# Optimization experiments

Hardware: AMD Instinct MI355X
Metric: run time of the kernel (lower is better)

Reference implementation:

```python
import jax, jax.numpy as jnp
import numpy as np

B, S, D_IN, H, BLOCKS, OUT_DIM = 32, 128, 16, 128, 3, 1
TAU = 0.5
BN_EPS = 1e-5


def _conv1d(x, w, b, dil):
    # x: [B, C, S], w: [O, I, K], 'same' padding with dilation (matches torch padding='same')
    y = jax.lax.conv_general_dilated(x, w, (1,), 'SAME', rhs_dilation=(dil,),
                                     dimension_numbers=('NCH', 'OIH', 'NCH'))
    return y + b[None, :, None]


def setup_inputs() -> dict:
    key = jax.random.key(0)
    ks = jax.random.split(key, 24)
    w = lambda k, shape, s=0.05: (jax.random.normal(k, shape, jnp.float32) * s)
    return {
        'data': jax.random.normal(ks[0], (B, S, D_IN), jnp.float32),
        'gumbel_u': jax.random.uniform(ks[1], (B, S * S, 2), jnp.float32),
        'w11': w(ks[2], (H, D_IN, 1)), 'b11': jnp.zeros((H,), jnp.float32),
        'w12': w(ks[3], (H, H, 3)),    'b12': jnp.zeros((H,), jnp.float32),
        'w21': w(ks[4], (H, D_IN, 1)), 'b21': jnp.zeros((H,), jnp.float32),
        'w22': w(ks[5], (H, H, 5)),    'b22': jnp.zeros((H,), jnp.float32),
        'w31': w(ks[6], (H, D_IN, 1)), 'b31': jnp.zeros((H,), jnp.float32),
        'wf': w(ks[7], (3 * H, H)),    'bf': jnp.zeros((H,), jnp.float32),
        'w1': w(ks[8], (2 * H, H)),    'b1': jnp.zeros((H,), jnp.float32),
        'w2': w(ks[9], (H, 2)),        'b2': jnp.zeros((2,), jnp.float32),
        'wl': w(ks[10], (BLOCKS, H, H)), 'bl': jnp.zeros((BLOCKS, H), jnp.float32),
        'wr': w(ks[11], (BLOCKS, H, H)),
        'gamma': jnp.ones((BLOCKS, H), jnp.float32), 'beta': jnp.zeros((BLOCKS, H), jnp.float32),
        'wg': w(ks[12], (BLOCKS, 1), 0.3), 'bg': jnp.zeros((1,), jnp.float32),
        'we': w(ks[13], (H, H // 2)),  'be': jnp.zeros((H // 2,), jnp.float32),
        'wo': w(ks[14], (H // 2, OUT_DIM)), 'bo': jnp.zeros((OUT_DIM,), jnp.float32),
    }


def reference(data, gumbel_u, w11, b11, w12, b12, w21, b21, w22, b22, w31, b31,
              wf, bf, w1, b1, w2, b2, wl, bl, wr, gamma, beta, wg, bg, we, be, wo, bo):
    b_, s_, _ = data.shape
    xd = jnp.transpose(data, (0, 2, 1))                    # [B, D_IN, S]
    # dilated TCN feature extraction
    x1 = _conv1d(_conv1d(xd, w11, b11, 1), w12, b12, 3)
    x2 = _conv1d(_conv1d(xd, w21, b21, 1), w22, b22, 5)
    x3 = _conv1d(xd, w31, b31, 1)
    x = jnp.concatenate([x1, x2, x3], axis=1)              # [B, 3H, S]
    x = jnp.transpose(x, (0, 2, 1))                        # [B, S, 3H]
    x = jax.nn.relu(x @ wf + bf)                           # [B, S, H] node features

    # edge scoring: pair (i,j) gets cat(sender=x[j], receiver=x[i]); fc1 split avoids [B,S,S,2H]
    hs = x @ w1[:H]                                        # sender part  [B, S, H]
    hr = x @ w1[H:]                                        # receiver part [B, S, H]
    h = jax.nn.relu(hs[:, None, :, :] + hr[:, :, None, :] + b1)  # [B, S(i), S(j), H]
    logits = h @ w2 + b2                                   # [B, S, S, 2]

    # hard gumbel-softmax, channel 0 = edge on
    u = jnp.clip(gumbel_u, 1e-6, 1.0 - 1e-6).reshape(b_, s_, s_, 2)
    g = -jnp.log(-jnp.log(u))
    y = (logits + g) / TAU
    adj = (jnp.argmax(y, axis=-1) == 0).astype(x.dtype)    # [B, S, S]
    # zero strict lower triangle (tri_mask) and diagonal (keep_self_loops=False)
    idx = jnp.arange(s_)
    adj = adj * (idx[None, :] > idx[:, None])[None]
    # edge_list in torch is non-differentiable -> no grad through adjacency
    adj = jax.lax.stop_gradient(adj)

    # SAGEConv (mean aggr) + BatchNorm, dense per-sample message passing
    deg = jnp.maximum(adj.sum(axis=1), 1.0)                # in-degree of target j, [B, S]
    xn = x
    outs = []
    for l in range(BLOCKS):
        agg = jnp.einsum('bij,bih->bjh', adj, xn) / deg[..., None]
        out = agg @ wl[l] + bl[l] + xn @ wr[l]             # lin_l(agg) + lin_r(x)
        m = out.mean(axis=(0, 1))
        v = out.var(axis=(0, 1))
        xn = (out - m) * jax.lax.rsqrt(v + BN_EPS) * gamma[l] + beta[l]
        outs.append(xn)

    stk = jnp.stack(outs, axis=-1)                          # [B, S, H, BLOCKS]
    xw = jax.nn.relu(jnp.einsum('bshk,ko->bsh', stk, wg) + bg[0])
    last = xw[:, -1]                                        # aggregate='last' -> [B, H]
    h2 = jax.nn.relu(last @ we + be)
    return h2 @ wo + bo                                     # [B, OUT_DIM]
```

## Files before the change

### kernel.cpp

```cpp
#include <hip/hip_runtime.h>
#include <math.h>

#define BB 32
#define SS 128
#define DIN 16
#define HH 128
#define NBSH (BB*SS*HH)

typedef __attribute__((ext_vector_type(8))) short short8;
typedef __attribute__((ext_vector_type(4))) float vf4;

__device__ __forceinline__ float4 f4fma(float s, float4 w, float4 c){
    return make_float4(fmaf(s,w.x,c.x), fmaf(s,w.y,c.y), fmaf(s,w.z,c.z), fmaf(s,w.w,c.w));
}
__device__ __forceinline__ unsigned short f2bf(float x){
    union { float f; unsigned int u; } v; v.f = x;
    unsigned int r = v.u + 0x7FFF + ((v.u >> 16) & 1);
    return (unsigned short)(r >> 16);
}
__device__ __forceinline__ float bf2f(unsigned short b){
    union { unsigned int u; float f; } v; v.u = ((unsigned int)b) << 16;
    return v.f;
}

__global__ __launch_bounds__(256) void k_prep(
    const float* __restrict__ w12, const float* __restrict__ w22,
    const float* __restrict__ w31,
    const float* __restrict__ w11, const float* __restrict__ b11,
    const float* __restrict__ w21, const float* __restrict__ b21,
    const float* __restrict__ wl, const float* __restrict__ wr,
    float* __restrict__ W3, float* __restrict__ W5, float* __restrict__ W31T,
    float* __restrict__ Beff1, float* __restrict__ Beff2, float* __restrict__ accf,
    unsigned short* __restrict__ wHi, unsigned short* __restrict__ wLo)
{
    __shared__ float W12L[8*384];
    __shared__ float W22L[8*640];
    __shared__ float w11L[2048], w21L[2048], b11L[128], b21L[128];
    int blk = blockIdx.x; int tid = threadIdx.x;

    if (blk < 16){
        int h0 = blk*8;
        for (int i = tid; i < 768; i += 256){
            int hl = i/96, o4 = i%96;
            *reinterpret_cast<float4*>(W12L + hl*384 + o4*4) =
                reinterpret_cast<const float4*>(w12)[(h0+hl)*96 + o4];
        }
        for (int i = tid; i < 1280; i += 256){
            int hl = i/160, o4 = i%160;
            *reinterpret_cast<float4*>(W22L + hl*640 + o4*4) =
                reinterpret_cast<const float4*>(w22)[(h0+hl)*160 + o4];
        }
        for (int i = tid; i < 512; i += 256)
            *reinterpret_cast<float4*>(w11L + i*4) = reinterpret_cast<const float4*>(w11)[i];
        for (int i = tid; i < 512; i += 256)
            *reinterpret_cast<float4*>(w21L + i*4) = reinterpret_cast<const float4*>(w21)[i];
        if (tid < 128){ b11L[tid] = b11[tid]; b21L[tid] = b21[tid]; }
        if (blk == 0){ for (int i = tid; i < 768; i += 256) accf[i] = 0.f; }
        __syncthreads();

        for (int T = tid; T < 1216; T += 256){
            if (T < 384){
                int hl = T/48, kd = T%48, k = kd>>4, d = kd&15;
                float a = 0.f;
                #pragma unroll 4
                for (int c = 0; c < HH; ++c) a = fmaf(W12L[hl*384 + c*3 + k], w11L[c*16 + d], a);
                W3[(k*16+d)*128 + h0+hl] = a;
            } else if (T < 1024){
                int tt = T-384, hl = tt/80, kd = tt%80, k = kd>>4, d = kd&15;
                float a = 0.f;
                #pragma unroll 4
                for (int c = 0; c < HH; ++c) a = fmaf(W22L[hl*640 + c*5 + k], w21L[c*16 + d], a);
                W5[(k*16+d)*128 + h0+hl] = a;
            } else if (T < 1048){
                int tt = T-1024, hl = tt/3, k = tt%3;
                float a = 0.f;
                #pragma unroll 4
                for (int c = 0; c < HH; ++c) a = fmaf(W12L[hl*384 + c*3 + k], b11L[c], a);
                Beff1[k*128 + h0+hl] = a;
            } else if (T < 1088){
                int tt = T-1048, hl = tt/5, k = tt%5;
                float a = 0.f;
                #pragma unroll 4
                for (int c = 0; c < HH; ++c) a = fmaf(W22L[hl*640 + c*5 + k], b21L[c], a);
                Beff2[k*128 + h0+hl] = a;
            } else {
                int tt = T-1088, hl = tt>>4, d = tt&15;
                W31T[d*128 + h0+hl] = w31[(h0+hl)*16 + d];
            }
        }
    } else {
        int q = blk - 16;
        int h = tid & 127; int half = tid >> 7;
        for (int rl = half; rl < 32; rl += 2){
            int r = q*32 + rl;
            int m = r >> 7;
            int c = r & 127;
            const float* src = (m < 3) ? (wl + (size_t)m*16384) : (wr + (size_t)(m-3)*16384);
            float v = src[c*128 + h];
            unsigned short hi = f2bf(v);
            unsigned short lo = f2bf(v - bf2f(hi));
            wHi[(size_t)m*16384 + h*128 + c] = hi;
            wLo[(size_t)m*16384 + h*128 + c] = lo;
        }
    }
}

__global__ __launch_bounds__(256) void k_fuse_all(
    const float* __restrict__ data,
    const float* __restrict__ W3, const float* __restrict__ W5,
    const float* __restrict__ W31T,
    const float* __restrict__ Beff1, const float* __restrict__ Beff2,
    const float* __restrict__ b12, const float* __restrict__ b22,
    const float* __restrict__ b31,
    const float* __restrict__ wf, const float* __restrict__ bf,
    const float* __restrict__ w1, const float* __restrict__ b1,
    float* __restrict__ hs, float* __restrict__ hrT, float* __restrict__ XT)
{
    __shared__ __align__(16) float sb[11648];
    float* At   = sb;
    float* Wt   = sb + 6912;
    float* dinT = sb + 11008;
    int blk = blockIdx.x; int row0 = blk*16;
    int b = row0 >> 7; int s0 = row0 & 127;
    int tid = threadIdx.x; int h = tid & 127; int g = tid >> 7;

    for (int idx = tid; idx < 576; idx += 256){
        int r = idx >> 4, d = idx & 15;
        int sp = s0 - 10 + r;
        dinT[d*40 + r] = (sp >= 0 && sp < SS) ? data[(b*SS+sp)*DIN + d] : 0.f;
    }
    __syncthreads();

    float a1[8], a2[8], a3[8];
    #pragma unroll
    for (int m = 0; m < 8; ++m){ a1[m]=0.f; a2[m]=0.f; a3[m]=0.f; }
    for (int d = 0; d < DIN; ++d){
        float w3v[3], w5v[5];
        #pragma unroll
        for (int k = 0; k < 3; ++k) w3v[k] = W3[(k*DIN+d)*HH + h];
        #pragma unroll
        for (int k = 0; k < 5; ++k) w5v[k] = W5[(k*DIN+d)*HH + h];
        float w31v = W31T[d*HH + h];
        const float* dp = dinT + d*40;
        #pragma unroll
        for (int sub = 0; sub < 2; ++sub){
            int rb = g*8 + sub*4;
            const float4* qp = reinterpret_cast<const float4*>(dp + rb);
            float4 q0=qp[0],q1=qp[1],q2=qp[2],q3=qp[3],q4=qp[4],q5=qp[5];
            float qf[24] = {q0.x,q0.y,q0.z,q0.w, q1.x,q1.y,q1.z,q1.w,
                            q2.x,q2.y,q2.z,q2.w, q3.x,q3.y,q3.z,q3.w,
                            q4.x,q4.y,q4.z,q4.w, q5.x,q5.y,q5.z,q5.w};
            #pragma unroll
            for (int tp = 0; tp < 4; ++tp){
                int m = sub*4 + tp;
                #pragma unroll
                for (int k = 0; k < 3; ++k) a1[m] = fmaf(qf[tp+3*k+7], w3v[k], a1[m]);
                #pragma unroll
                for (int k = 0; k < 5; ++k) a2[m] = fmaf(qf[tp+5*k], w5v[k], a2[m]);
                a3[m] = fmaf(qf[tp+10], w31v, a3[m]);
            }
        }
    }
    {
        float be1[3] = {Beff1[h], Beff1[HH+h], Beff1[2*HH+h]};
        float be2[5] = {Beff2[h], Beff2[HH+h], Beff2[2*HH+h], Beff2[3*HH+h], Beff2[4*HH+h]};
        float bv12 = b12[h], bv22 = b22[h], bv31 = b31[h];
        #pragma unroll
        for (int m = 0; m < 8; ++m){
            int rl = g*8 + m;
            int s = s0 + rl;
            float v1 = a1[m] + bv12;
            #pragma unroll
            for (int k = 0; k < 3; ++k)
                if ((unsigned)(s + 3*k - 3) < SS) v1 += be1[k];
            float v2 = a2[m] + bv22;
            #pragma unroll
            for (int k = 0; k < 5; ++k)
                if ((unsigned)(s + 5*k - 10) < SS) v2 += be2[k];
            At[h*18 + rl]        = v1;
            At[(HH+h)*18 + rl]   = v2;
            At[(2*HH+h)*18 + rl] = a3[m] + bv31;
        }
    }
    __syncthreads();

    int r0 = (tid>>5)*2, c0 = (tid&31)*4;
    float4 facc[2] = {{0,0,0,0},{0,0,0,0}};
    for (int ch = 0; ch < 12; ++ch){
        int kk0 = ch*32;
        #pragma unroll
        for (int u = 0; u < 4; ++u){
            int k = (tid>>5) + 8*u;
            *reinterpret_cast<float4*>(Wt + k*128 + c0) =
                *reinterpret_cast<const float4*>(wf + (size_t)(kk0+k)*128 + c0);
        }
        __syncthreads();
        #pragma unroll 4
        for (int k = 0; k < 32; ++k){
            float2 a = *reinterpret_cast<const float2*>(At + (kk0+k)*18 + r0);
            float4 w = *reinterpret_cast<const float4*>(Wt + k*128 + c0);
            facc[0] = f4fma(a.x, w, facc[0]);
            facc[1] = f4fma(a.y, w, facc[1]);
        }
        __syncthreads();
    }
    float* xT = sb;
    float* Wb = sb + 2304;
    float* Wa = sb + 6912;
    {
        float4 bf4 = *reinterpret_cast<const float4*>(bf + c0);
        #pragma unroll
        for (int u = 0; u < 2; ++u){
            float4 v = make_float4(fmaxf(facc[u].x+bf4.x,0.f), fmaxf(facc[u].y+bf4.y,0.f),
                                   fmaxf(facc[u].z+bf4.z,0.f), fmaxf(facc[u].w+bf4.w,0.f));
            xT[(c0+0)*18 + r0+u] = v.x;
            xT[(c0+1)*18 + r0+u] = v.y;
            xT[(c0+2)*18 + r0+u] = v.z;
            xT[(c0+3)*18 + r0+u] = v.w;
        }
    }
    __syncthreads();

    float4 as[2] = {{0,0,0,0},{0,0,0,0}};
    float4 ar[2] = {{0,0,0,0},{0,0,0,0}};
    for (int ch = 0; ch < 4; ++ch){
        int ck0 = ch*32;
        #pragma unroll
        for (int u = 0; u < 4; ++u){
            int k = (tid>>5) + 8*u;
            *reinterpret_cast<float4*>(Wa + k*128 + c0) =
                *reinterpret_cast<const float4*>(w1 + (size_t)(ck0+k)*128 + c0);
            *reinterpret_cast<float4*>(Wb + k*128 + c0) =
                *reinterpret_cast<const float4*>(w1 + (size_t)(128+ck0+k)*128 + c0);
        }
        __syncthreads();
        #pragma unroll 4
        for (int k = 0; k < 32; ++k){
            float2 a = *reinterpret_cast<const float2*>(xT + (ck0+k)*18 + r0);
            float4 wa = *reinterpret_cast<const float4*>(Wa + k*128 + c0);
            float4 wb = *reinterpret_cast<const float4*>(Wb + k*128 + c0);
            as[0]=f4fma(a.x,wa,as[0]); ar[0]=f4fma(a.x,wb,ar[0]);
            as[1]=f4fma(a.y,wa,as[1]); ar[1]=f4fma(a.y,wb,ar[1]);
        }
        __syncthreads();
    }
    float4 b14 = *reinterpret_cast<const float4*>(b1 + c0);
    int rin = s0 + r0;
    #pragma unroll
    for (int u = 0; u < 2; ++u){
        *reinterpret_cast<float4*>(hs + (size_t)(row0+r0+u)*128 + c0) =
            make_float4(as[u].x, as[u].y, as[u].z, as[u].w);
        hrT[((size_t)b*HH + c0+0)*SS + rin+u] = ar[u].x + b14.x;
        hrT[((size_t)b*HH + c0+1)*SS + rin+u] = ar[u].y + b14.y;
        hrT[((size_t)b*HH + c0+2)*SS + rin+u] = ar[u].z + b14.z;
        hrT[((size_t)b*HH + c0+3)*SS + rin+u] = ar[u].w + b14.w;
    }
    for (int idx = tid; idx < 2048; idx += 256){
        int c = idx >> 4, s = idx & 15;
        XT[((size_t)(b*HH + c))*SS + s0 + s] = xT[c*18 + s];
    }
}

__global__ __launch_bounds__(256) void k_adj(
    const float* __restrict__ hs, const float* __restrict__ hrT,
    const float* __restrict__ w2, const float* __restrict__ b2,
    const float* __restrict__ gu, unsigned short* __restrict__ adjT,
    float* __restrict__ deginv)
{
    int blk = blockIdx.x; int b = blk >> 4; int j0 = (blk & 15) * 8;
    int tid = threadIdx.x; int i = tid & 127; int g = tid >> 7;
    __shared__ float hsL[8][128];
    __shared__ float w20L[128], w21L[128];
    __shared__ int degS[8];
    for (int idx = tid; idx < 1024; idx += 256){
        int jj = idx >> 7, h = idx & 127;
        hsL[jj][h] = hs[(size_t)(b*SS + j0 + jj)*HH + h];
    }
    if (tid < 128){ w20L[tid] = w2[tid*2]; w21L[tid] = w2[tid*2+1]; }
    if (tid < 8) degS[tid] = 0;
    __syncthreads();
    float d0[4] = {0,0,0,0}, d1[4] = {0,0,0,0};
    const float* hrb = hrT + (size_t)b*HH*SS + i;
    #pragma unroll 4
    for (int h = 0; h < 128; ++h){
        float hrv = hrb[(size_t)h*SS];
        float wa = w20L[h], wb = w21L[h];
        float r0 = fmaxf(hsL[g*4+0][h] + hrv, 0.f);
        float r1 = fmaxf(hsL[g*4+1][h] + hrv, 0.f);
        float r2 = fmaxf(hsL[g*4+2][h] + hrv, 0.f);
        float r3 = fmaxf(hsL[g*4+3][h] + hrv, 0.f);
        d0[0]=fmaf(r0,wa,d0[0]); d1[0]=fmaf(r0,wb,d1[0]);
        d0[1]=fmaf(r1,wa,d0[1]); d1[1]=fmaf(r1,wb,d1[1]);
        d0[2]=fmaf(r2,wa,d0[2]); d1[2]=fmaf(r2,wb,d1[2]);
        d0[3]=fmaf(r3,wa,d0[3]); d1[3]=fmaf(r3,wb,d1[3]);
    }
    float b20 = b2[0], b21 = b2[1];
    #pragma unroll
    for (int jj = 0; jj < 4; ++jj){
        int j = j0 + g*4 + jj;
        size_t e = (size_t)(b*SS + i)*SS + j;
        float2 uv = *reinterpret_cast<const float2*>(gu + e*2);
        float u0 = fminf(fmaxf(uv.x, 1e-6f), 0.999999f);
        float u1 = fminf(fmaxf(uv.y, 1e-6f), 0.999999f);
        float g0 = -logf(-logf(u0));
        float g1 = -logf(-logf(u1));
        float y0 = d0[jj] + b20 + g0;
        float y1 = d1[jj] + b21 + g1;
        bool av = (j > i) && (y0 >= y1);
        adjT[(size_t)(b*SS + j)*SS + i] = av ? (unsigned short)0x3F80 : (unsigned short)0;
        unsigned long long msk = __ballot(av);
        if ((tid & 63) == 0) atomicAdd(&degS[g*4+jj], (int)__popcll(msk));
    }
    __syncthreads();
    if (tid < 8) deginv[b*SS + j0 + tid] = 1.f / fmaxf((float)degS[tid], 1.f);
}

#define AGGH 0
#define AGGL 4352
#define ADJA 8704
#define XH   13056
#define XL   22272
#define LINA 8704
#define XNJH 29184
#define XNJL 33536
__global__ __launch_bounds__(512) void k_gnn(
    const unsigned short* __restrict__ adjT, const float* __restrict__ xnT,
    const float* __restrict__ deginv,
    const float* __restrict__ gammaP, const float* __restrict__ betaP,
    const float* __restrict__ accP, int aff,
    const unsigned short* __restrict__ wlH, const unsigned short* __restrict__ wlL,
    const unsigned short* __restrict__ wrH, const unsigned short* __restrict__ wrL,
    const float* __restrict__ bl,
    float* __restrict__ outT, float* __restrict__ accL)
{
    __shared__ __align__(16) unsigned short pool[37888];
    __shared__ float2 scsh[128];
    __shared__ float dinvL[32];
    __shared__ float2 redS[128];
    __shared__ float blL[128];
    int blk = blockIdx.x; int b = blk >> 2; int j0 = (blk & 3) * 32;
    int tid = threadIdx.x; int lane = tid & 63; int w = tid >> 6;
    int frow = lane & 15, fk = (lane >> 4) * 8;

    if (tid < 128){
        if (aff){
            float2 s = reinterpret_cast<const float2*>(accP)[tid];
            float m = s.x * (1.f/4096.f);
            float var = fmaxf(s.y * (1.f/4096.f) - m*m, 0.f);
            float sc = gammaP[tid] / sqrtf(var + 1e-5f);
            scsh[tid] = make_float2(sc, betaP[tid] - m*sc);
        } else scsh[tid] = make_float2(1.f, 0.f);
        redS[tid] = make_float2(0.f, 0.f);
        blL[tid] = bl[tid];
    }
    if (tid < 32) dinvL[tid] = deginv[b*SS + j0 + tid];
    __syncthreads();

    {
        int jl = tid >> 4, c8 = tid & 15;
        *reinterpret_cast<uint4*>(pool + ADJA + jl*136 + c8*8) =
            *reinterpret_cast<const uint4*>(adjT + ((size_t)(b*SS + j0 + jl))*SS + c8*8);
    }

    int mt = w & 1, ntb = (w >> 1) * 2;
    vf4 acc[2]; acc[0]=0.f; acc[1]=0.f;
    for (int cs = 0; cs < 2; ++cs){
        for (int task = tid; task < 2048; task += 512){
            int hh = task >> 4, q = task & 15;
            float4 v = *reinterpret_cast<const float4*>(
                xnT + ((size_t)(b*HH + hh))*SS + cs*64 + q*4);
            float2 ss = scsh[hh];
            float e0 = fmaf(v.x, ss.x, ss.y), e1 = fmaf(v.y, ss.x, ss.y);
            float e2 = fmaf(v.z, ss.x, ss.y), e3 = fmaf(v.w, ss.x, ss.y);
            unsigned short h0 = f2bf(e0), h1 = f2bf(e1), h2 = f2bf(e2), h3 = f2bf(e3);
            unsigned int hA = (unsigned int)h0 | ((unsigned int)h1 << 16);
            unsigned int hB = (unsigned int)h2 | ((unsigned int)h3 << 16);
            unsigned short l0 = f2bf(e0 - bf2f(h0)), l1 = f2bf(e1 - bf2f(h1));
            unsigned short l2 = f2bf(e2 - bf2f(h2)), l3 = f2bf(e3 - bf2f(h3));
            unsigned int lA = (unsigned int)l0 | ((unsigned int)l1 << 16);
            unsigned int lB = (unsigned int)l2 | ((unsigned int)l3 << 16);
            *reinterpret_cast<uint2*>(pool + XH + hh*72 + q*4) = make_uint2(hA, hB);
            *reinterpret_cast<uint2*>(pool + XL + hh*72 + q*4) = make_uint2(lA, lB);
        }
        __syncthreads();
        #pragma unroll
        for (int ks = 0; ks < 2; ++ks){
            short8 af = *reinterpret_cast<const short8*>(
                pool + ADJA + (mt*16 + frow)*136 + cs*64 + ks*32 + fk);
            #pragma unroll
            for (int ntl = 0; ntl < 2; ++ntl){
                int nt = ntb + ntl;
                short8 bh = *reinterpret_cast<const short8*>(
                    pool + XH + (nt*16 + frow)*72 + ks*32 + fk);
                short8 bo = *reinterpret_cast<const short8*>(
                    pool + XL + (nt*16 + frow)*72 + ks*32 + fk);
                acc[ntl] = __builtin_amdgcn_mfma_f32_16x16x32_bf16(af, bh, acc[ntl], 0, 0, 0);
                acc[ntl] = __builtin_amdgcn_mfma_f32_16x16x32_bf16(af, bo, acc[ntl], 0, 0, 0);
            }
        }
        __syncthreads();
    }
    #pragma unroll
    for (int ntl = 0; ntl < 2; ++ntl){
        int hh = (ntb + ntl)*16 + frow;
        #pragma unroll
        for (int r = 0; r < 4; ++r){
            int jl = mt*16 + (lane>>4)*4 + r;
            float v = acc[ntl][r] * dinvL[jl];
            unsigned short hi = f2bf(v);
            pool[AGGH + jl*136 + hh] = hi;
            pool[AGGL + jl*136 + hh] = f2bf(v - bf2f(hi));
        }
    }
    if (tid < 256){
        int jg = tid >> 5, cg = tid & 31;
        float mv[4][4];
        #pragma unroll
        for (int e = 0; e < 4; ++e){
            float4 v = *reinterpret_cast<const float4*>(
                xnT + ((size_t)(b*HH + cg*4 + e))*SS + j0 + jg*4);
            float2 ss = scsh[cg*4 + e];
            mv[e][0]=fmaf(v.x,ss.x,ss.y); mv[e][1]=fmaf(v.y,ss.x,ss.y);
            mv[e][2]=fmaf(v.z,ss.x,ss.y); mv[e][3]=fmaf(v.w,ss.x,ss.y);
        }
        #pragma unroll
        for (int f = 0; f < 4; ++f){
            int jl = jg*4 + f;
            unsigned short h0=f2bf(mv[0][f]), h1=f2bf(mv[1][f]), h2=f2bf(mv[2][f]), h3=f2bf(mv[3][f]);
            unsigned int a0 = (unsigned int)h0 | ((unsigned int)h1<<16);
            unsigned int a1v = (unsigned int)h2 | ((unsigned int)h3<<16);
            unsigned short l0=f2bf(mv[0][f]-bf2f(h0)), l1=f2bf(mv[1][f]-bf2f(h1));
            unsigned short l2=f2bf(mv[2][f]-bf2f(h2)), l3=f2bf(mv[3][f]-bf2f(h3));
            unsigned int b0 = (unsigned int)l0 | ((unsigned int)l1<<16);
            unsigned int b1v = (unsigned int)l2 | ((unsigned int)l3<<16);
            *reinterpret_cast<uint2*>(pool + XNJH + jl*136 + cg*4) = make_uint2(a0, a1v);
            *reinterpret_cast<uint2*>(pool + XNJL + jl*136 + cg*4) = make_uint2(b0, b1v);
        }
    }
    __syncthreads();

    vf4 lacc[2]; lacc[0]=0.f; lacc[1]=0.f;
    const unsigned short* wptr[4] = {wlH, wlL, wrH, wrL};
    for (int ck = 0; ck < 4; ++ck){
        for (int task = tid; task < 2048; task += 512){
            int mat = task >> 9, hh = (task >> 2) & 127, q = task & 3;
            *reinterpret_cast<uint4*>(pool + LINA + mat*5120 + hh*40 + q*8) =
                *reinterpret_cast<const uint4*>(wptr[mat] + (size_t)hh*128 + ck*32 + q*8);
        }
        __syncthreads();
        #pragma unroll
        for (int mat = 0; mat < 2; ++mat){
            int Ah = LINA + (mat*2)*5120;
            int Al = LINA + (mat*2+1)*5120;
            int Bh = mat ? XNJH : AGGH;
            int Bl = mat ? XNJL : AGGL;
            short8 ah = *reinterpret_cast<const short8*>(pool + Ah + (w*16 + frow)*40 + fk);
            short8 al = *reinterpret_cast<const short8*>(pool + Al + (w*16 + frow)*40 + fk);
            #pragma unroll
            for (int ntl = 0; ntl < 2; ++ntl){
                short8 bh = *reinterpret_cast<const short8*>(
                    pool + Bh + (ntl*16 + frow)*136 + ck*32 + fk);
                short8 bo = *reinterpret_cast<const short8*>(
                    pool + Bl + (ntl*16 + frow)*136 + ck*32 + fk);
                lacc[ntl] = __builtin_amdgcn_mfma_f32_16x16x32_bf16(ah, bh, lacc[ntl], 0,0,0);
                lacc[ntl] = __builtin_amdgcn_mfma_f32_16x16x32_bf16(ah, bo, lacc[ntl], 0,0,0);
                lacc[ntl] = __builtin_amdgcn_mfma_f32_16x16x32_bf16(al, bh, lacc[ntl], 0,0,0);
            }
        }
        __syncthreads();
    }
    #pragma unroll
    for (int ntl = 0; ntl < 2; ++ntl){
        #pragma unroll
        for (int r = 0; r < 4; ++r){
            int hh = w*16 + (lane>>4)*4 + r;
            int jl = ntl*16 + (lane & 15);
            float v = lacc[ntl][r] + blL[hh];
            outT[((size_t)(b*HH + hh))*SS + j0 + jl] = v;
            float s1 = v, s2 = v*v;
            #pragma unroll
            for (int off = 1; off < 16; off <<= 1){
                s1 += __shfl_xor(s1, off, 64);
                s2 += __shfl_xor(s2, off, 64);
            }
            if ((lane & 15) == 0){ redS[hh].x += s1; redS[hh].y += s2; }
        }
    }
    __syncthreads();
    if (tid < 128){
        atomicAdd(&accL[2*tid],   redS[tid].x);
        atomicAdd(&accL[2*tid+1], redS[tid].y);
    }
}

__global__ __launch_bounds__(128) void k_head(
    const float* __restrict__ t0, const float* __restrict__ t1,
    const float* __restrict__ t2, const float* __restrict__ accf,
    const float* __restrict__ gamma, const float* __restrict__ beta,
    const float* __restrict__ wg, const float* __restrict__ bg,
    const float* __restrict__ we, const float* __restrict__ be,
    const float* __restrict__ wo, const float* __restrict__ bo,
    float* __restrict__ out)
{
    int b = blockIdx.x; int t = threadIdx.x;
    __shared__ float xw[HH];
    const float* outs[3] = {t0, t1, t2};
    float a = bg[0];
    #pragma unroll
    for (int l = 0; l < 3; ++l){
        float2 s = reinterpret_cast<const float2*>(accf)[l*128 + t];
        float m = s.x * (1.f/4096.f);
        float var = fmaxf(s.y * (1.f/4096.f) - m*m, 0.f);
        float sc = gamma[l*128+t] / sqrtf(var + 1e-5f);
        float sh = beta[l*128+t] - m*sc;
        float val = fmaf(outs[l][((size_t)(b*HH + t))*SS + SS-1], sc, sh);
        a = fmaf(val, wg[l], a);
    }
    xw[t] = fmaxf(a, 0.f);
    __syncthreads();
    if (t < 64){
        float acc = be[t];
        for (int h = 0; h < HH; ++h) acc = fmaf(xw[h], we[h*64 + t], acc);
        float h2 = fmaxf(acc, 0.f);
        float r = h2 * wo[t];
        #pragma unroll
        for (int off = 32; off; off >>= 1) r += __shfl_down(r, off, 64);
        if (t == 0) out[b] = r + bo[0];
    }
}

extern "C" void kernel_launch(void* const* d_in, const int* in_sizes, int n_in,
                              void* d_out, int out_size, void* d_ws, size_t ws_size,
                              hipStream_t stream)
{
    const float* data = (const float*)d_in[0];
    const float* gu   = (const float*)d_in[1];
    const float* w11  = (const float*)d_in[2];
    const float* b11  = (const float*)d_in[3];
    const float* w12  = (const float*)d_in[4];
    const float* b12  = (const float*)d_in[5];
    const float* w21  = (const float*)d_in[6];
    const float* b21  = (const float*)d_in[7];
    const float* w22  = (const float*)d_in[8];
    const float* b22  = (const float*)d_in[9];
    const float* w31  = (const float*)d_in[10];
    const float* b31  = (const float*)d_in[11];
    const float* wf   = (const float*)d_in[12];
    const float* bf   = (const float*)d_in[13];
    const float* w1   = (const float*)d_in[14];
    const float* b1   = (const float*)d_in[15];
    const float* w2   = (const float*)d_in[16];
    const float* b2   = (const float*)d_in[17];
    const float* wl   = (const float*)d_in[18];
    const float* bl   = (const float*)d_in[19];
    const float* wr   = (const float*)d_in[20];
    const float* gamma= (const float*)d_in[21];
    const float* beta = (const float*)d_in[22];
    const float* wg   = (const float*)d_in[23];
    const float* bg   = (const float*)d_in[24];
    const float* we   = (const float*)d_in[25];
    const float* be   = (const float*)d_in[26];
    const float* wo   = (const float*)d_in[27];
    const float* bo   = (const float*)d_in[28];
    float* out = (float*)d_out;

    float* ws = (float*)d_ws;
    float* hs   = ws;
    float* hrT  = ws + (size_t)NBSH;
    float* XT   = ws + (size_t)2*NBSH;
    float* T0   = ws + (size_t)3*NBSH;
    float* T1   = ws + (size_t)4*NBSH;
    float* T2   = ws + (size_t)5*NBSH;
    float* G    = ws + (size_t)6*NBSH;
    float* W3    = G;
    float* W5    = G + 6144;
    float* W31T  = G + 16384;
    float* Beff1 = G + 18432;
    float* Beff2 = G + 18816;
    float* accf  = G + 19456;
    float* dinv  = G + 20224;
    unsigned short* adjTG = (unsigned short*)(G + 24320);
    unsigned short* wHi   = (unsigned short*)(G + 24320 + 262144);
    unsigned short* wLo   = (unsigned short*)(G + 24320 + 262144 + 49152);

    k_prep<<<40, 256, 0, stream>>>(w12, w22, w31, w11, b11, w21, b21, wl, wr,
                                   W3, W5, W31T, Beff1, Beff2, accf, wHi, wLo);
    k_fuse_all<<<256, 256, 0, stream>>>(data, W3, W5, W31T, Beff1, Beff2,
                                        b12, b22, b31, wf, bf, w1, b1,
                                        hs, hrT, XT);
    k_adj<<<512, 256, 0, stream>>>(hs, hrT, w2, b2, gu, adjTG, dinv);

    const float* xnTs[3] = {XT, T0, T1};
    float*       outs[3] = {T0, T1, T2};
    for (int l = 0; l < 3; ++l){
        int aff = (l > 0);
        const float* gP = gamma + (l>0 ? (l-1)*HH : 0);
        const float* bP = beta  + (l>0 ? (l-1)*HH : 0);
        const float* aP = accf + (l>0 ? (l-1)*256 : 0);
        k_gnn<<<128, 512, 0, stream>>>(adjTG, xnTs[l], dinv, gP, bP, aP, aff,
            wHi + (size_t)l*16384, wLo + (size_t)l*16384,
            wHi + (size_t)(3+l)*16384, wLo + (size_t)(3+l)*16384,
            bl + (size_t)l*HH, outs[l], accf + (size_t)l*256);
    }
    k_head<<<BB, 128, 0, stream>>>(T0, T1, T2, accf, gamma, beta,
                                   wg, bg, we, be, wo, bo, out);
}
```

Before: 141.9 us.

## Run fusion and MLP projections in k_fuse_all on bf16x3 MFMA

Converts the wf and w1 weights into transposed bf16 hi/lo pairs in k_prep using extra blocks. k_fuse_all now runs at 512 threads and computes the 384->128 fusion GEMM and both halves of the w1 projection with 16x16x32 bf16 MFMA, using a split-precision scheme (hi*hi + hi*lo + lo*hi + lo*lo) instead of scalar FP32 FMA loops. The goal is to cut the dominant FMA cost of the per-row GEMMs. The cost is extra prep work and bf16 split rounding, and the x activations are now stored as the sum of their hi and lo parts rather than exact fp32.

```diff
diff --git a/kernel.cpp b/kernel.cpp
--- a/kernel.cpp
+++ b/kernel.cpp
@@ -10,9 +10,6 @@
 typedef __attribute__((ext_vector_type(8))) short short8;
 typedef __attribute__((ext_vector_type(4))) float vf4;
 
-__device__ __forceinline__ float4 f4fma(float s, float4 w, float4 c){
-    return make_float4(fmaf(s,w.x,c.x), fmaf(s,w.y,c.y), fmaf(s,w.z,c.z), fmaf(s,w.w,c.w));
-}
 __device__ __forceinline__ unsigned short f2bf(float x){
     union { float f; unsigned int u; } v; v.f = x;
     unsigned int r = v.u + 0x7FFF + ((v.u >> 16) & 1);
@@ -29,13 +26,18 @@
     const float* __restrict__ w11, const float* __restrict__ b11,
     const float* __restrict__ w21, const float* __restrict__ b21,
     const float* __restrict__ wl, const float* __restrict__ wr,
+    const float* __restrict__ wf, const float* __restrict__ w1,
     float* __restrict__ W3, float* __restrict__ W5, float* __restrict__ W31T,
     float* __restrict__ Beff1, float* __restrict__ Beff2, float* __restrict__ accf,
-    unsigned short* __restrict__ wHi, unsigned short* __restrict__ wLo)
+    unsigned short* __restrict__ wHi, unsigned short* __restrict__ wLo,
+    unsigned short* __restrict__ wfTH, unsigned short* __restrict__ wfTL,
+    unsigned short* __restrict__ w1sTH, unsigned short* __restrict__ w1sTL,
+    unsigned short* __restrict__ w1rTH, unsigned short* __restrict__ w1rTL)
 {
     __shared__ float W12L[8*384];
     __shared__ float W22L[8*640];
     __shared__ float w11L[2048], w21L[2048], b11L[128], b21L[128];
+    __shared__ float S[4096];
     int blk = blockIdx.x; int tid = threadIdx.x;
 
     if (blk < 16){
@@ -88,7 +90,7 @@
                 W31T[d*128 + h0+hl] = w31[(h0+hl)*16 + d];
             }
         }
-    } else {
+    } else if (blk < 40){
         int q = blk - 16;
         int h = tid & 127; int half = tid >> 7;
         for (int rl = half; rl < 32; rl += 2){
@@ -102,38 +104,64 @@
             wHi[(size_t)m*16384 + h*128 + c] = hi;
             wLo[(size_t)m*16384 + h*128 + c] = lo;
         }
-    }
-}
-
-__global__ __launch_bounds__(256) void k_fuse_all(
+    } else {
+        int t2 = blk - 40;
+        const float* src; unsigned short *dH, *dL; int kbase, rstride;
+        if (t2 < 12){ src = wf + (size_t)t2*32*128; dH = wfTH; dL = wfTL; kbase = t2*32; rstride = 384; }
+        else if (t2 < 16){ int c = t2-12; src = w1 + (size_t)c*32*128; dH = w1sTH; dL = w1sTL; kbase = c*32; rstride = 128; }
+        else { int c = t2-16; src = w1 + 16384 + (size_t)c*32*128; dH = w1rTH; dL = w1rTL; kbase = c*32; rstride = 128; }
+        for (int i = tid; i < 1024; i += 256)
+            reinterpret_cast<float4*>(S)[i] = reinterpret_cast<const float4*>(src)[i];
+        __syncthreads();
+        for (int task = tid; task < 4096; task += 256){
+            int h = task & 127, kl = task >> 7;
+            float v = S[kl*128 + h];
+            unsigned short hi = f2bf(v);
+            dH[(size_t)h*rstride + kbase + kl] = hi;
+            dL[(size_t)h*rstride + kbase + kl] = f2bf(v - bf2f(hi));
+        }
+    }
+}
+
+#define AHo 0
+#define ALo 6272
+#define BHo 12544
+#define BLo 17664
+#define xHo 22784
+#define xLo 24960
+__global__ __launch_bounds__(512) void k_fuse_all(
     const float* __restrict__ data,
     const float* __restrict__ W3, const float* __restrict__ W5,
     const float* __restrict__ W31T,
     const float* __restrict__ Beff1, const float* __restrict__ Beff2,
     const float* __restrict__ b12, const float* __restrict__ b22,
     const float* __restrict__ b31,
-    const float* __restrict__ wf, const float* __restrict__ bf,
-    const float* __restrict__ w1, const float* __restrict__ b1,
+    const unsigned short* __restrict__ wfTH, const unsigned short* __restrict__ wfTL,
+    const float* __restrict__ bf,
+    const unsigned short* __restrict__ w1sTH, const unsigned short* __restrict__ w1sTL,
+    const unsigned short* __restrict__ w1rTH, const unsigned short* __restrict__ w1rTL,
+    const float* __restrict__ b1,
     float* __restrict__ hs, float* __restrict__ hrT, float* __restrict__ XT)
 {
-    __shared__ __align__(16) float sb[11648];
-    float* At   = sb;
-    float* Wt   = sb + 6912;
-    float* dinT = sb + 11008;
+    __shared__ __align__(16) unsigned short pool[27136];
+    __shared__ __align__(16) float dinT[16*40];
+    __shared__ float bfL[128], b1L[128];
     int blk = blockIdx.x; int row0 = blk*16;
     int b = row0 >> 7; int s0 = row0 & 127;
-    int tid = threadIdx.x; int h = tid & 127; int g = tid >> 7;
-
-    for (int idx = tid; idx < 576; idx += 256){
+    int tid = threadIdx.x; int lane = tid & 63; int w = tid >> 6;
+    int h = tid & 127; int quarter = tid >> 7;
+    int frow = lane & 15, fk = (lane >> 4) * 8;
+
+    for (int idx = tid; idx < 576; idx += 512){
         int r = idx >> 4, d = idx & 15;
         int sp = s0 - 10 + r;
         dinT[d*40 + r] = (sp >= 0 && sp < SS) ? data[(b*SS+sp)*DIN + d] : 0.f;
     }
-    __syncthreads();
-
-    float a1[8], a2[8], a3[8];
-    #pragma unroll
-    for (int m = 0; m < 8; ++m){ a1[m]=0.f; a2[m]=0.f; a3[m]=0.f; }
+    if (tid < 128){ bfL[tid] = bf[tid]; b1L[tid] = b1[tid]; }
+    __syncthreads();
+
+    float a1[4] = {0,0,0,0}, a2[4] = {0,0,0,0}, a3[4] = {0,0,0,0};
+    int rb = quarter*4;
     for (int d = 0; d < DIN; ++d){
         float w3v[3], w5v[5];
         #pragma unroll
@@ -141,24 +169,18 @@
         #pragma unroll
         for (int k = 0; k < 5; ++k) w5v[k] = W5[(k*DIN+d)*HH + h];
         float w31v = W31T[d*HH + h];
-        const float* dp = dinT + d*40;
-        #pragma unroll
-        for (int sub = 0; sub < 2; ++sub){
-            int rb = g*8 + sub*4;
-            const float4* qp = reinterpret_cast<const float4*>(dp + rb);
-            float4 q0=qp[0],q1=qp[1],q2=qp[2],q3=qp[3],q4=qp[4],q5=qp[5];
-            float qf[24] = {q0.x,q0.y,q0.z,q0.w, q1.x,q1.y,q1.z,q1.w,
-                            q2.x,q2.y,q2.z,q2.w, q3.x,q3.y,q3.z,q3.w,
-                            q4.x,q4.y,q4.z,q4.w, q5.x,q5.y,q5.z,q5.w};
+        const float4* qp = reinterpret_cast<const float4*>(dinT + d*40 + rb);
+        float4 q0=qp[0],q1=qp[1],q2=qp[2],q3=qp[3],q4=qp[4],q5=qp[5];
+        float qf[24] = {q0.x,q0.y,q0.z,q0.w, q1.x,q1.y,q1.z,q1.w,
+                        q2.x,q2.y,q2.z,q2.w, q3.x,q3.y,q3.z,q3.w,
+                        q4.x,q4.y,q4.z,q4.w, q5.x,q5.y,q5.z,q5.w};
+        #pragma unroll
+        for (int tp = 0; tp < 4; ++tp){
             #pragma unroll
-            for (int tp = 0; tp < 4; ++tp){
-                int m = sub*4 + tp;
-                #pragma unroll
-                for (int k = 0; k < 3; ++k) a1[m] = fmaf(qf[tp+3*k+7], w3v[k], a1[m]);
-                #pragma unroll
-                for (int k = 0; k < 5; ++k) a2[m] = fmaf(qf[tp+5*k], w5v[k], a2[m]);
-                a3[m] = fmaf(qf[tp+10], w31v, a3[m]);
-            }
+            for (int k = 0; k < 3; ++k) a1[tp] = fmaf(qf[tp+3*k+7], w3v[k], a1[tp]);
+            #pragma unroll
+            for (int k = 0; k < 5; ++k) a2[tp] = fmaf(qf[tp+5*k], w5v[k], a2[tp]);
+            a3[tp] = fmaf(qf[tp+10], w31v, a3[tp]);
         }
     }
     {
@@ -166,98 +188,105 @@
         float be2[5] = {Beff2[h], Beff2[HH+h], Beff2[2*HH+h], Beff2[3*HH+h], Beff2[4*HH+h]};
         float bv12 = b12[h], bv22 = b22[h], bv31 = b31[h];
         #pragma unroll
-        for (int m = 0; m < 8; ++m){
-            int rl = g*8 + m;
+        for (int tp = 0; tp < 4; ++tp){
+            int rl = rb + tp;
             int s = s0 + rl;
-            float v1 = a1[m] + bv12;
+            float v1 = a1[tp] + bv12;
             #pragma unroll
             for (int k = 0; k < 3; ++k)
                 if ((unsigned)(s + 3*k - 3) < SS) v1 += be1[k];
-            float v2 = a2[m] + bv22;
+            float v2 = a2[tp] + bv22;
             #pragma unroll
             for (int k = 0; k < 5; ++k)
                 if ((unsigned)(s + 5*k - 10) < SS) v2 += be2[k];
-            At[h*18 + rl]        = v1;
-            At[(HH+h)*18 + rl]   = v2;
-            At[(2*HH+h)*18 + rl] = a3[m] + bv31;
-        }
-    }
-    __syncthreads();
-
-    int r0 = (tid>>5)*2, c0 = (tid&31)*4;
-    float4 facc[2] = {{0,0,0,0},{0,0,0,0}};
+            float v3 = a3[tp] + bv31;
+            unsigned short h1 = f2bf(v1), h2 = f2bf(v2), h3 = f2bf(v3);
+            pool[AHo + rl*392 + h]        = h1;
+            pool[AHo + rl*392 + 128 + h]  = h2;
+            pool[AHo + rl*392 + 256 + h]  = h3;
+            pool[ALo + rl*392 + h]        = f2bf(v1 - bf2f(h1));
+            pool[ALo + rl*392 + 128 + h]  = f2bf(v2 - bf2f(h2));
+            pool[ALo + rl*392 + 256 + h]  = f2bf(v3 - bf2f(h3));
+        }
+    }
+    __syncthreads();
+
+    vf4 facc; facc = 0.f;
     for (int ch = 0; ch < 12; ++ch){
-        int kk0 = ch*32;
-        #pragma unroll
-        for (int u = 0; u < 4; ++u){
-            int k = (tid>>5) + 8*u;
-            *reinterpret_cast<float4*>(Wt + k*128 + c0) =
-                *reinterpret_cast<const float4*>(wf + (size_t)(kk0+k)*128 + c0);
-        }
-        __syncthreads();
-        #pragma unroll 4
-        for (int k = 0; k < 32; ++k){
-            float2 a = *reinterpret_cast<const float2*>(At + (kk0+k)*18 + r0);
-            float4 w = *reinterpret_cast<const float4*>(Wt + k*128 + c0);
-            facc[0] = f4fma(a.x, w, facc[0]);
-            facc[1] = f4fma(a.y, w, facc[1]);
-        }
-        __syncthreads();
-    }
-    float* xT = sb;
-    float* Wb = sb + 2304;
-    float* Wa = sb + 6912;
+        int ck0 = ch*32;
+        for (int task = tid; task < 1024; task += 512){
+            int isL = task >> 9; int n = (task >> 2) & 127; int q = task & 3;
+            const unsigned short* srcw = isL ? wfTL : wfTH;
+            unsigned short* dst = pool + (isL ? BLo : BHo);
+            *reinterpret_cast<uint4*>(dst + n*40 + q*8) =
+                *reinterpret_cast<const uint4*>(srcw + (size_t)n*384 + ck0 + q*8);
+        }
+        __syncthreads();
+        short8 ah = *reinterpret_cast<const short8*>(pool + AHo + frow*392 + ck0 + fk);
+        short8 al = *reinterpret_cast<const short8*>(pool + ALo + frow*392 + ck0 + fk);
+        short8 bh = *reinterpret_cast<const short8*>(pool + BHo + (w*16+frow)*40 + fk);
+        short8 bl = *reinterpret_cast<const short8*>(pool + BLo + (w*16+frow)*40 + fk);
+        facc = __builtin_amdgcn_mfma_f32_16x16x32_bf16(ah, bh, facc, 0,0,0);
+        facc = __builtin_amdgcn_mfma_f32_16x16x32_bf16(ah, bl, facc, 0,0,0);
+        facc = __builtin_amdgcn_mfma_f32_16x16x32_bf16(al, bh, facc, 0,0,0);
+        facc = __builtin_amdgcn_mfma_f32_16x16x32_bf16(al, bl, facc, 0,0,0);
+        __syncthreads();
+    }
     {
-        float4 bf4 = *reinterpret_cast<const float4*>(bf + c0);
-        #pragma unroll
-        for (int u = 0; u < 2; ++u){
-            float4 v = make_float4(fmaxf(facc[u].x+bf4.x,0.f), fmaxf(facc[u].y+bf4.y,0.f),
-                                   fmaxf(facc[u].z+bf4.z,0.f), fmaxf(facc[u].w+bf4.w,0.f));
-            xT[(c0+0)*18 + r0+u] = v.x;
-            xT[(c0+1)*18 + r0+u] = v.y;
-            xT[(c0+2)*18 + r0+u] = v.z;
-            xT[(c0+3)*18 + r0+u] = v.w;
-        }
-    }
-    __syncthreads();
-
-    float4 as[2] = {{0,0,0,0},{0,0,0,0}};
-    float4 ar[2] = {{0,0,0,0},{0,0,0,0}};
-    for (int ch = 0; ch < 4; ++ch){
-        int ck0 = ch*32;
-        #pragma unroll
-        for (int u = 0; u < 4; ++u){
-            int k = (tid>>5) + 8*u;
-            *reinterpret_cast<float4*>(Wa + k*128 + c0) =
-                *reinterpret_cast<const float4*>(w1 + (size_t)(ck0+k)*128 + c0);
-            *reinterpret_cast<float4*>(Wb + k*128 + c0) =
-                *reinterpret_cast<const float4*>(w1 + (size_t)(128+ck0+k)*128 + c0);
-        }
-        __syncthreads();
-        #pragma unroll 4
-        for (int k = 0; k < 32; ++k){
-            float2 a = *reinterpret_cast<const float2*>(xT + (ck0+k)*18 + r0);
-            float4 wa = *reinterpret_cast<const float4*>(Wa + k*128 + c0);
-            float4 wb = *reinterpret_cast<const float4*>(Wb + k*128 + c0);
-            as[0]=f4fma(a.x,wa,as[0]); ar[0]=f4fma(a.x,wb,ar[0]);
-            as[1]=f4fma(a.y,wa,as[1]); ar[1]=f4fma(a.y,wb,ar[1]);
-        }
-        __syncthreads();
-    }
-    float4 b14 = *reinterpret_cast<const float4*>(b1 + c0);
-    int rin = s0 + r0;
-    #pragma unroll
-    for (int u = 0; u < 2; ++u){
-        *reinterpret_cast<float4*>(hs + (size_t)(row0+r0+u)*128 + c0) =
-            make_float4(as[u].x, as[u].y, as[u].z, as[u].w);
-        hrT[((size_t)b*HH + c0+0)*SS + rin+u] = ar[u].x + b14.x;
-        hrT[((size_t)b*HH + c0+1)*SS + rin+u] = ar[u].y + b14.y;
-        hrT[((size_t)b*HH + c0+2)*SS + rin+u] = ar[u].z + b14.z;
-        hrT[((size_t)b*HH + c0+3)*SS + rin+u] = ar[u].w + b14.w;
-    }
-    for (int idx = tid; idx < 2048; idx += 256){
-        int c = idx >> 4, s = idx & 15;
-        XT[((size_t)(b*HH + c))*SS + s0 + s] = xT[c*18 + s];
+        int n_col = w*16 + (lane & 15);
+        float bfv = bfL[n_col];
+        #pragma unroll
+        for (int r = 0; r < 4; ++r){
+            int m = (lane>>4)*4 + r;
+            float v = fmaxf(facc[r] + bfv, 0.f);
+            unsigned short hi = f2bf(v);
+            pool[xHo + m*136 + n_col] = hi;
+            pool[xLo + m*136 + n_col] = f2bf(v - bf2f(hi));
+        }
+    }
+    __syncthreads();
+    for (int task = tid; task < 2048; task += 512){
+        int m = task & 15, c = task >> 4;
+        float v = bf2f(pool[xHo + m*136 + c]) + bf2f(pool[xLo + m*136 + c]);
+        XT[((size_t)(b*HH + c))*SS + s0 + m] = v;
+    }
+
+    vf4 as, ar; as = 0.f; ar = 0.f;
+    for (int pass = 0; pass < 2; ++pass){
+        const unsigned short* sH = pass ? w1rTH : w1sTH;
+        const unsigned short* sL = pass ? w1rTL : w1sTL;
+        vf4 acc; acc = 0.f;
+        for (int ch = 0; ch < 4; ++ch){
+            int ck0 = ch*32;
+            for (int task = tid; task < 1024; task += 512){
+                int isL = task >> 9; int n = (task >> 2) & 127; int q = task & 3;
+                const unsigned short* srcw = isL ? sL : sH;
+                unsigned short* dst = pool + (isL ? BLo : BHo);
+                *reinterpret_cast<uint4*>(dst + n*40 + q*8) =
+                    *reinterpret_cast<const uint4*>(srcw + (size_t)n*128 + ck0 + q*8);
+            }
+            __syncthreads();
+            short8 ah = *reinterpret_cast<const short8*>(pool + xHo + frow*136 + ck0 + fk);
+            short8 al = *reinterpret_cast<const short8*>(pool + xLo + frow*136 + ck0 + fk);
+            short8 bh = *reinterpret_cast<const short8*>(pool + BHo + (w*16+frow)*40 + fk);
+            short8 bl = *reinterpret_cast<const short8*>(pool + BLo + (w*16+frow)*40 + fk);
+            acc = __builtin_amdgcn_mfma_f32_16x16x32_bf16(ah, bh, acc, 0,0,0);
+            acc = __builtin_amdgcn_mfma_f32_16x16x32_bf16(ah, bl, acc, 0,0,0);
+            acc = __builtin_amdgcn_mfma_f32_16x16x32_bf16(al, bh, acc, 0,0,0);
+            acc = __builtin_amdgcn_mfma_f32_16x16x32_bf16(al, bl, acc, 0,0,0);
+            __syncthreads();
+        }
+        if (pass == 0) as = acc; else ar = acc;
+    }
+    {
+        int n_col = w*16 + (lane & 15);
+        float b1v = b1L[n_col];
+        #pragma unroll
+        for (int r = 0; r < 4; ++r){
+            int m = (lane>>4)*4 + r;
+            hs[(size_t)(row0+m)*128 + n_col] = as[r];
+            hrT[((size_t)(b*HH + n_col))*SS + s0 + m] = ar[r] + b1v;
+        }
     }
 }
 
@@ -580,13 +609,22 @@
     float* accf  = G + 19456;
     float* dinv  = G + 20224;
     unsigned short* adjTG = (unsigned short*)(G + 24320);
-    unsigned short* wHi   = (unsigned short*)(G + 24320 + 262144);
-    unsigned short* wLo   = (unsigned short*)(G + 24320 + 262144 + 49152);
-
-    k_prep<<<40, 256, 0, stream>>>(w12, w22, w31, w11, b11, w21, b21, wl, wr,
-                                   W3, W5, W31T, Beff1, Beff2, accf, wHi, wLo);
-    k_fuse_all<<<256, 256, 0, stream>>>(data, W3, W5, W31T, Beff1, Beff2,
-                                        b12, b22, b31, wf, bf, w1, b1,
+    unsigned short* wHi   = (unsigned short*)(G + 286464);
+    unsigned short* wLo   = (unsigned short*)(G + 335616);
+    unsigned short* wfTH  = (unsigned short*)(G + 384768);
+    unsigned short* wfTL  = (unsigned short*)(G + 409344);
+    unsigned short* w1sTH = (unsigned short*)(G + 433920);
+    unsigned short* w1sTL = (unsigned short*)(G + 442112);
+    unsigned short* w1rTH = (unsigned short*)(G + 450304);
+    unsigned short* w1rTL = (unsigned short*)(G + 458496);
+
+    k_prep<<<60, 256, 0, stream>>>(w12, w22, w31, w11, b11, w21, b21, wl, wr,
+                                   wf, w1,
+                                   W3, W5, W31T, Beff1, Beff2, accf, wHi, wLo,
+                                   wfTH, wfTL, w1sTH, w1sTL, w1rTH, w1rTL);
+    k_fuse_all<<<256, 512, 0, stream>>>(data, W3, W5, W31T, Beff1, Beff2,
+                                        b12, b22, b31,
+                                        wfTH, wfTL, bf, w1sTH, w1sTL, w1rTH, w1rTL, b1,
                                         hs, hrT, XT);
     k_adj<<<512, 256, 0, stream>>>(hs, hrT, w2, b2, gu, adjTG, dinv);
 
```

Result: faster. 130.6 us (-8.0%).
